# Kernel tuning notes

Hardware: AMD Instinct MI355X
Metric: run time of the kernel (lower is better)

## Reference

```python
import jax, jax.numpy as jnp
import numpy as np

N, LQ, C, M, L, P = 8, 2048, 256, 8, 4, 4
DH = C // M  # 32
LENS = (2048, 1024, 512, 256)


def setup_inputs() -> dict:
    key = jax.random.key(0)
    ks = jax.random.split(key, 8)
    s = 1.0 / np.sqrt(C)
    return {
        "query": jax.random.normal(ks[0], (N, LQ, C), jnp.float32),
        "reference_points": jax.random.uniform(ks[1], (N, LQ, L, 1), jnp.float32),
        "input_flatten": jax.random.normal(ks[2], (N, sum(LENS), C), jnp.float32),
        "temporal_lens": np.array(LENS, np.int64),
        "level_start_index": np.array([0, 2048, 3072, 3584], np.int64),
        "W_off": jax.random.normal(ks[3], (C, M * L * P), jnp.float32) * 0.01,
        "b_off": jax.random.normal(ks[4], (M * L * P,), jnp.float32),
        "W_attn": jax.random.normal(ks[5], (C, M * L * P), jnp.float32) * 0.01,
        "b_attn": jnp.zeros((M * L * P,), jnp.float32),
        "W_val": jax.random.normal(ks[6], (C, C), jnp.float32) * s,
        "b_val": jnp.zeros((C,), jnp.float32),
        "W_out": jax.random.normal(ks[7], (C, C), jnp.float32) * s,
        "b_out": jnp.zeros((C,), jnp.float32),
    }


def _deform_core(value, lens, loc, attn):
    # value: (N, S, M, DH); loc, attn: (N, LQ, M, L, P); loc in normalized [0,1] coords.
    # Equivalent to per-level F.grid_sample (bilinear, zeros padding, align_corners=False)
    # on a 1xT image: pixel position = loc*T - 0.5; the y-coord 0.5 lands exactly on row 0.
    outs = []
    start = 0
    for l, T in enumerate(lens):
        v = value[:, start:start + T].transpose(0, 2, 1, 3)  # (N, M, T, DH)
        start += T
        pos = loc[..., l, :] * T - 0.5                       # (N, LQ, M, P)
        x0f = jnp.floor(pos)
        frac = pos - x0f
        x0 = x0f.astype(jnp.int32)

        def gather(idx):
            i = jnp.clip(idx, 0, T - 1).transpose(0, 2, 1, 3).reshape(N, M, LQ * P, 1)
            return jnp.take_along_axis(v, i, axis=2).reshape(N, M, LQ, P, DH)

        in0 = ((x0 >= 0) & (x0 < T)).astype(value.dtype)
        in1 = ((x0 + 1 >= 0) & (x0 + 1 < T)).astype(value.dtype)
        w0 = ((1.0 - frac) * in0).transpose(0, 2, 1, 3)[..., None]  # (N, M, LQ, P, 1)
        w1 = (frac * in1).transpose(0, 2, 1, 3)[..., None]
        outs.append(gather(x0) * w0 + gather(x0 + 1) * w1)          # (N, M, LQ, P, DH)
    sampled = jnp.stack(outs, axis=3)          # (N, M, LQ, L, P, DH)
    aw = attn.transpose(0, 2, 1, 3, 4)         # (N, M, LQ, L, P)
    return jnp.einsum('nmqlpd,nmqlp->nqmd', sampled, aw).reshape(N, LQ, C)


def reference(query, reference_points, input_flatten, temporal_lens, level_start_index,
              W_off, b_off, W_attn, b_attn, W_val, b_val, W_out, b_out):
    lens = [int(t) for t in np.asarray(temporal_lens)[:L]]  # static per-level lengths
    value = (input_flatten @ W_val + b_val).reshape(N, -1, M, DH)
    off = (query @ W_off + b_off).reshape(N, LQ, M, L, P)
    attn = jax.nn.softmax((query @ W_attn + b_attn).reshape(N, LQ, M, L * P), axis=-1)
    attn = attn.reshape(N, LQ, M, L, P)
    norm = jnp.asarray(lens, query.dtype)                    # offset_normalizer (L,)
    loc = reference_points[:, :, None, :, None, 0] + off / norm[None, None, None, :, None]
    out = _deform_core(value, lens, loc, attn)
    out = out @ W_out + b_out
    return out, loc, attn
```

## Files before the change

### kernel.cpp

```cpp
#include <hip/hip_runtime.h>
#include <hip/hip_bf16.h>
#include <math.h>

#define NB 8
#define LQ 2048
#define SSUM 3840

typedef unsigned short ushort_t;
typedef unsigned int uint_t;
typedef __attribute__((ext_vector_type(8))) short bf16x8;
typedef __attribute__((ext_vector_type(4))) float f32x4;

__device__ __forceinline__ ushort_t f2bf(float f) {
  __hip_bfloat16 h = __float2bfloat16(f);
  return *reinterpret_cast<ushort_t*>(&h);
}
__device__ __forceinline__ uint_t pk2bf(float lo, float hi) {
  float2 t; t.x = lo; t.y = hi;
  __hip_bfloat162 h = __float22bfloat162_rn(t);
  return *reinterpret_cast<uint_t*>(&h);
}
__device__ __forceinline__ float bf2f_lo(uint_t u) {
  union { uint_t u32; float f; } x;
  x.u32 = u << 16;
  return x.f;
}
__device__ __forceinline__ float bf2f_hi(uint_t u) {
  union { uint_t u32; float f; } x;
  x.u32 = u & 0xffff0000u;
  return x.f;
}
__device__ __forceinline__ void ld_lds16(const void* g, void* l) {
  __builtin_amdgcn_global_load_lds(
      (const __attribute__((address_space(1))) void*)g,
      (__attribute__((address_space(3))) void*)l, 16, 0, 0);
}

#define NF4A ((NB * SSUM * 256) / 4)
#define NF4B ((NB * LQ * 256) / 4)

__global__ __launch_bounds__(256) void prologue(
    const float* __restrict__ in_flat, const float* __restrict__ query,
    const float* __restrict__ W_val, const float* __restrict__ W_off,
    const float* __restrict__ W_attn, const float* __restrict__ W_out,
    ushort_t* __restrict__ inflat_bf, ushort_t* __restrict__ query_bf,
    ushort_t* __restrict__ BtVal, ushort_t* __restrict__ BtOA,
    ushort_t* __restrict__ BtOut) {
  const int b = blockIdx.x, t = threadIdx.x;
  if (b < 256) { BtVal[b * 256 + t] = f2bf(W_val[(size_t)t * 256 + b]); return; }
  if (b < 512) { int n = b - 256; BtOut[n * 256 + t] = f2bf(W_out[(size_t)t * 256 + n]); return; }
  if (b < 640) { int n = b - 512; BtOA[n * 256 + t] = f2bf(W_off[(size_t)t * 128 + n]); return; }
  if (b < 768) { int n = b - 640; BtOA[(128 + n) * 256 + t] = f2bf(W_attn[(size_t)t * 128 + n]); return; }
  const int stride = (gridDim.x - 768) * 256;
  for (int i = (b - 768) * 256 + t; i < NF4A + NF4B; i += stride) {
    float4 v;
    if (i < NF4A) v = ((const float4*)in_flat)[i];
    else          v = ((const float4*)query)[i - NF4A];
    uint2 o;
    o.x = pk2bf(v.x, v.y);
    o.y = pk2bf(v.z, v.w);
    if (i < NF4A) *(uint2*)&inflat_bf[(size_t)i * 4] = o;
    else          *(uint2*)&query_bf[(size_t)(i - NF4A) * 4] = o;
  }
}

__global__ __launch_bounds__(256) void gemm_async(
    int job_base,
    const ushort_t* __restrict__ inflat_bf, const ushort_t* __restrict__ query_bf,
    const ushort_t* __restrict__ core,
    const ushort_t* __restrict__ BtVal, const ushort_t* __restrict__ BtOA,
    const ushort_t* __restrict__ BtOut,
    const float* __restrict__ b_val, const float* __restrict__ b_off,
    const float* __restrict__ b_attn, const float* __restrict__ b_out,
    ushort_t* __restrict__ value, float* __restrict__ loc,
    float* __restrict__ attn, float* __restrict__ out) {
  __shared__ ushort_t Ab[2][64][32];
  __shared__ ushort_t Bb[2][128][32];

  const int job = job_base + blockIdx.x;

  const ushort_t* Asrc; const ushort_t* Bt; const float* bias;
  int bm, colbase, cstride;
  ushort_t* Cb = nullptr; float* Cf = nullptr;

  if (job < 960) {
    int cn = job & 1; bm = (job >> 1) * 64;
    Asrc = inflat_bf; Bt = BtVal + cn * 128 * 256;
    bias = b_val + cn * 128; Cb = value; cstride = 256; colbase = cn * 128;
  } else if (job < 1472) {
    int p = job - 960; int cn = p & 1; bm = (p >> 1) * 64;
    Asrc = query_bf; Bt = BtOA + cn * 128 * 256;
    bias = cn ? b_attn : b_off; Cf = cn ? attn : loc; cstride = 128; colbase = 0;
  } else {
    int o = job - 1472; int cn = o & 1; bm = (o >> 1) * 64;
    Asrc = core; Bt = BtOut + cn * 128 * 256;
    bias = b_out + cn * 128; Cf = out; cstride = 256; colbase = cn * 128;
  }

  const int tid = threadIdx.x;
  const int lane = tid & 63;
  const int wv = tid >> 6;
  const int quad = lane >> 4;
  const int l16 = lane & 15;
  const int wm = (wv >> 1) * 32;
  const int wn = (wv & 1) * 64;
  const int srow = lane >> 2;
  const int skb = (lane & 3) * 8;

  f32x4 acc[2][4];
#pragma unroll
  for (int i = 0; i < 2; ++i)
#pragma unroll
    for (int j = 0; j < 4; ++j) acc[i][j] = (f32x4)(0.f);

  auto stage = [&](int db, int k0) {
    ld_lds16(Asrc + (size_t)(bm + wv * 16 + srow) * 256 + k0 + skb,
             &Ab[db][wv * 16 + srow][skb]);
    ld_lds16(Bt + (size_t)(wv * 32 + srow) * 256 + k0 + skb,
             &Bb[db][wv * 32 + srow][skb]);
    ld_lds16(Bt + (size_t)(wv * 32 + 16 + srow) * 256 + k0 + skb,
             &Bb[db][wv * 32 + 16 + srow][skb]);
  };

  stage(0, 0);
#pragma unroll
  for (int it = 0; it < 8; ++it) {
    const int db = it & 1;
    __syncthreads();
    if (it < 7) stage(db ^ 1, (it + 1) * 32);
    bf16x8 af[2], bfr[4];
#pragma unroll
    for (int mi = 0; mi < 2; ++mi)
      af[mi] = *(const bf16x8*)&Ab[db][wm + mi * 16 + l16][quad * 8];
#pragma unroll
    for (int ni = 0; ni < 4; ++ni)
      bfr[ni] = *(const bf16x8*)&Bb[db][wn + ni * 16 + l16][quad * 8];
#pragma unroll
    for (int mi = 0; mi < 2; ++mi)
#pragma unroll
      for (int ni = 0; ni < 4; ++ni)
        acc[mi][ni] = __builtin_amdgcn_mfma_f32_16x16x32_bf16(af[mi], bfr[ni], acc[mi][ni], 0, 0, 0);
  }

#pragma unroll
  for (int ni = 0; ni < 4; ++ni) {
    int lc = wn + ni * 16 + l16;
    float bv = bias[lc];
    int cc = colbase + lc;
#pragma unroll
    for (int mi = 0; mi < 2; ++mi) {
      f32x4 v = acc[mi][ni];
      int rbase = bm + wm + mi * 16 + quad * 4;
#pragma unroll
      for (int r = 0; r < 4; ++r) {
        float o = v[r] + bv;
        size_t idx = (size_t)(rbase + r) * cstride + cc;
        if (Cb) Cb[idx] = f2bf(o);
        else    Cf[idx] = o;
      }
    }
  }
}

__global__ __launch_bounds__(256) void deform_fused(
    const ushort_t* __restrict__ value,
    float* __restrict__ locbuf,
    float* __restrict__ attnbuf,
    const float* __restrict__ refp,
    ushort_t* __restrict__ core) {
  const int tid = threadIdx.x;
  const int nq0 = blockIdx.x * 4;
  const int n = nq0 >> 11;

  __shared__ float slv[512];
  __shared__ float slog[512];
  __shared__ float4 sp[512];

  const float rnorm[4] = {1.f / 2048.f, 1.f / 1024.f, 1.f / 512.f, 1.f / 256.f};
  const int lensA[4] = {2048, 1024, 512, 256};
  const int startsA[4] = {0, 2048, 3072, 3584};

#pragma unroll
  for (int j = 0; j < 2; ++j) {
    int s = tid + j * 256;
    int q = s >> 7;
    int r = s & 127;
    int l = (r >> 2) & 3;
    float lv = refp[(size_t)(nq0 + q) * 4 + l] +
               locbuf[(size_t)nq0 * 128 + s] * rnorm[l];
    locbuf[(size_t)nq0 * 128 + s] = lv;
    slv[s] = lv;
    slog[s] = attnbuf[(size_t)nq0 * 128 + s];
  }
  __syncthreads();

  if (tid < 32) {
    int base = tid * 16;
    float v[16];
#pragma unroll
    for (int i = 0; i < 16; ++i) v[i] = slog[base + i];
    float mx = v[0];
#pragma unroll
    for (int i = 1; i < 16; ++i) mx = fmaxf(mx, v[i]);
    float ssum = 0.f;
#pragma unroll
    for (int i = 0; i < 16; ++i) { v[i] = __expf(v[i] - mx); ssum += v[i]; }
    float rs = 1.f / ssum;
    float* gout = attnbuf + (size_t)nq0 * 128 + base;
#pragma unroll
    for (int i = 0; i < 16; ++i) {
      float pv = v[i] * rs;
      slog[base + i] = pv;
      gout[i] = pv;
    }
  }
  __syncthreads();

#pragma unroll
  for (int j = 0; j < 2; ++j) {
    int s = tid + j * 256;
    int q = s >> 7;
    int r = s & 127;
    int m = r >> 4;
    int lp = r & 15;
    int l = lp >> 2;
    int T = lensA[l];
    float lv = slv[s];
    float aw = slog[s];
    float pos = lv * (float)T - 0.5f;
    float x0f = floorf(pos);
    float fr = pos - x0f;
    int x0 = (int)x0f;
    float w0 = ((unsigned)x0 < (unsigned)T) ? (1.f - fr) * aw : 0.f;
    float w1 = ((unsigned)(x0 + 1) < (unsigned)T) ? fr * aw : 0.f;
    int i0 = min(max(x0, 0), T - 1);
    int i1 = min(max(x0 + 1, 0), T - 1);
    float4 pr;
    pr.x = w0;
    pr.y = w1;
    pr.z = __int_as_float((startsA[l] + i0) * 256);
    pr.w = __int_as_float((startsA[l] + i1) * 256);
    sp[q * 128 + lp * 8 + m] = pr;
  }
  __syncthreads();

  const int q = tid >> 6;
  const int t64 = tid & 63;
  const int m = t64 >> 3;
  const int g = t64 & 7;
  const ushort_t* vbase = value + (size_t)n * (SSUM * 256) + m * 32 + g * 4;

  float a0 = 0.f, a1 = 0.f, a2 = 0.f, a3 = 0.f;
#pragma unroll
  for (int lp = 0; lp < 16; ++lp) {
    float4 pr = sp[q * 128 + lp * 8 + m];
    int o0 = __float_as_int(pr.z);
    int o1 = __float_as_int(pr.w);
    uint2 u0 = *(const uint2*)(vbase + o0);
    uint2 u1 = *(const uint2*)(vbase + o1);
    a0 += pr.x * bf2f_lo(u0.x) + pr.y * bf2f_lo(u1.x);
    a1 += pr.x * bf2f_hi(u0.x) + pr.y * bf2f_hi(u1.x);
    a2 += pr.x * bf2f_lo(u0.y) + pr.y * bf2f_lo(u1.y);
    a3 += pr.x * bf2f_hi(u0.y) + pr.y * bf2f_hi(u1.y);
  }
  uint2 outp;
  outp.x = (uint_t)f2bf(a0) | ((uint_t)f2bf(a1) << 16);
  outp.y = (uint_t)f2bf(a2) | ((uint_t)f2bf(a3) << 16);
  *(uint2*)&core[(size_t)(nq0 + q) * 256 + m * 32 + g * 4] = outp;
}

extern "C" void kernel_launch(void* const* d_in, const int* in_sizes, int n_in,
                              void* d_out, int out_size, void* d_ws, size_t ws_size,
                              hipStream_t stream) {
  const float* query    = (const float*)d_in[0];
  const float* refpts   = (const float*)d_in[1];
  const float* in_flat  = (const float*)d_in[2];
  const float* W_off  = (const float*)d_in[5];
  const float* b_off  = (const float*)d_in[6];
  const float* W_attn = (const float*)d_in[7];
  const float* b_attn = (const float*)d_in[8];
  const float* W_val  = (const float*)d_in[9];
  const float* b_val  = (const float*)d_in[10];
  const float* W_out  = (const float*)d_in[11];
  const float* b_out  = (const float*)d_in[12];

  float* out  = (float*)d_out;
  float* loc  = out + (size_t)NB * LQ * 256;
  float* attn = loc + (size_t)NB * LQ * 128;

  ushort_t* value     = (ushort_t*)d_ws;
  ushort_t* inflat_bf = value + (size_t)NB * SSUM * 256;
  ushort_t* query_bf  = inflat_bf + (size_t)NB * SSUM * 256;
  ushort_t* core      = query_bf;
  ushort_t* BtVal     = query_bf + (size_t)NB * LQ * 256;
  ushort_t* BtOA      = BtVal + 65536;
  ushort_t* BtOut     = BtOA + 65536;

  const int Mq = NB * LQ;

  prologue<<<768 + 2048, 256, 0, stream>>>(
      in_flat, query, W_val, W_off, W_attn, W_out,
      inflat_bf, query_bf, BtVal, BtOA, BtOut);

  gemm_async<<<1472, 256, 0, stream>>>(
      0, inflat_bf, query_bf, core, BtVal, BtOA, BtOut,
      b_val, b_off, b_attn, b_out, value, loc, attn, out);

  deform_fused<<<Mq / 4, 256, 0, stream>>>(value, loc, attn, refpts, core);

  gemm_async<<<512, 256, 0, stream>>>(
      1472, inflat_bf, query_bf, core, BtVal, BtOA, BtOut,
      b_val, b_off, b_attn, b_out, value, loc, attn, out);
}
```

Baseline: 174.5 us.

## Fuse fp32-to-bf16 activation conversion into GEMM with direct register loads

Removes the separate bulk conversion pass that wrote bf16 copies of input_flatten and query. The GEMM now reads fp32 activations straight from global memory and converts them to bf16 in registers. It also drops the LDS double-buffered async staging, so every wave loads its own A and B fragments from global memory. This saves one full read and write of the activations, but it loses LDS data sharing between waves, so global and L2 traffic for B and A rises, and the loads are no longer overlapped with compute.

Result: slower. 199.9 us (+14.6%).

```diff
diff --git a/kernel.cpp b/kernel.cpp
--- a/kernel.cpp
+++ b/kernel.cpp
@@ -30,43 +30,22 @@
   x.u32 = u & 0xffff0000u;
   return x.f;
 }
-__device__ __forceinline__ void ld_lds16(const void* g, void* l) {
-  __builtin_amdgcn_global_load_lds(
-      (const __attribute__((address_space(1))) void*)g,
-      (__attribute__((address_space(3))) void*)l, 16, 0, 0);
-}
-
-#define NF4A ((NB * SSUM * 256) / 4)
-#define NF4B ((NB * LQ * 256) / 4)
-
-__global__ __launch_bounds__(256) void prologue(
-    const float* __restrict__ in_flat, const float* __restrict__ query,
+
+__global__ __launch_bounds__(256) void prep(
     const float* __restrict__ W_val, const float* __restrict__ W_off,
     const float* __restrict__ W_attn, const float* __restrict__ W_out,
-    ushort_t* __restrict__ inflat_bf, ushort_t* __restrict__ query_bf,
     ushort_t* __restrict__ BtVal, ushort_t* __restrict__ BtOA,
     ushort_t* __restrict__ BtOut) {
   const int b = blockIdx.x, t = threadIdx.x;
   if (b < 256) { BtVal[b * 256 + t] = f2bf(W_val[(size_t)t * 256 + b]); return; }
   if (b < 512) { int n = b - 256; BtOut[n * 256 + t] = f2bf(W_out[(size_t)t * 256 + n]); return; }
   if (b < 640) { int n = b - 512; BtOA[n * 256 + t] = f2bf(W_off[(size_t)t * 128 + n]); return; }
-  if (b < 768) { int n = b - 640; BtOA[(128 + n) * 256 + t] = f2bf(W_attn[(size_t)t * 128 + n]); return; }
-  const int stride = (gridDim.x - 768) * 256;
-  for (int i = (b - 768) * 256 + t; i < NF4A + NF4B; i += stride) {
-    float4 v;
-    if (i < NF4A) v = ((const float4*)in_flat)[i];
-    else          v = ((const float4*)query)[i - NF4A];
-    uint2 o;
-    o.x = pk2bf(v.x, v.y);
-    o.y = pk2bf(v.z, v.w);
-    if (i < NF4A) *(uint2*)&inflat_bf[(size_t)i * 4] = o;
-    else          *(uint2*)&query_bf[(size_t)(i - NF4A) * 4] = o;
-  }
-}
-
-__global__ __launch_bounds__(256) void gemm_async(
+  int n = b - 640; BtOA[(128 + n) * 256 + t] = f2bf(W_attn[(size_t)t * 128 + n]);
+}
+
+__global__ __launch_bounds__(256) void gemm_reg(
     int job_base,
-    const ushort_t* __restrict__ inflat_bf, const ushort_t* __restrict__ query_bf,
+    const float* __restrict__ in_flat, const float* __restrict__ query,
     const ushort_t* __restrict__ core,
     const ushort_t* __restrict__ BtVal, const ushort_t* __restrict__ BtOA,
     const ushort_t* __restrict__ BtOut,
@@ -74,26 +53,25 @@
     const float* __restrict__ b_attn, const float* __restrict__ b_out,
     ushort_t* __restrict__ value, float* __restrict__ loc,
     float* __restrict__ attn, float* __restrict__ out) {
-  __shared__ ushort_t Ab[2][64][32];
-  __shared__ ushort_t Bb[2][128][32];
-
   const int job = job_base + blockIdx.x;
 
-  const ushort_t* Asrc; const ushort_t* Bt; const float* bias;
+  const float* Afp = nullptr;
+  const ushort_t* Abf = nullptr;
+  const ushort_t* Bt; const float* bias;
   int bm, colbase, cstride;
   ushort_t* Cb = nullptr; float* Cf = nullptr;
 
   if (job < 960) {
     int cn = job & 1; bm = (job >> 1) * 64;
-    Asrc = inflat_bf; Bt = BtVal + cn * 128 * 256;
+    Afp = in_flat; Bt = BtVal + cn * 128 * 256;
     bias = b_val + cn * 128; Cb = value; cstride = 256; colbase = cn * 128;
   } else if (job < 1472) {
     int p = job - 960; int cn = p & 1; bm = (p >> 1) * 64;
-    Asrc = query_bf; Bt = BtOA + cn * 128 * 256;
+    Afp = query; Bt = BtOA + cn * 128 * 256;
     bias = cn ? b_attn : b_off; Cf = cn ? attn : loc; cstride = 128; colbase = 0;
   } else {
     int o = job - 1472; int cn = o & 1; bm = (o >> 1) * 64;
-    Asrc = core; Bt = BtOut + cn * 128 * 256;
+    Abf = core; Bt = BtOut + cn * 128 * 256;
     bias = b_out + cn * 128; Cf = out; cstride = 256; colbase = cn * 128;
   }
 
@@ -104,8 +82,13 @@
   const int l16 = lane & 15;
   const int wm = (wv >> 1) * 32;
   const int wn = (wv & 1) * 64;
-  const int srow = lane >> 2;
-  const int skb = (lane & 3) * 8;
+
+  const size_t arow0 = (size_t)(bm + wm + l16) * 256 + quad * 8;
+  const size_t arow1 = arow0 + 16 * 256;
+  const ushort_t* bcol[4];
+#pragma unroll
+  for (int ni = 0; ni < 4; ++ni)
+    bcol[ni] = Bt + (size_t)(wn + ni * 16 + l16) * 256 + quad * 8;
 
   f32x4 acc[2][4];
 #pragma unroll
@@ -113,28 +96,32 @@
 #pragma unroll
     for (int j = 0; j < 4; ++j) acc[i][j] = (f32x4)(0.f);
 
-  auto stage = [&](int db, int k0) {
-    ld_lds16(Asrc + (size_t)(bm + wv * 16 + srow) * 256 + k0 + skb,
-             &Ab[db][wv * 16 + srow][skb]);
-    ld_lds16(Bt + (size_t)(wv * 32 + srow) * 256 + k0 + skb,
-             &Bb[db][wv * 32 + srow][skb]);
-    ld_lds16(Bt + (size_t)(wv * 32 + 16 + srow) * 256 + k0 + skb,
-             &Bb[db][wv * 32 + 16 + srow][skb]);
-  };
-
-  stage(0, 0);
-#pragma unroll
-  for (int it = 0; it < 8; ++it) {
-    const int db = it & 1;
-    __syncthreads();
-    if (it < 7) stage(db ^ 1, (it + 1) * 32);
+  union cvt_t { uint4 u; bf16x8 v; };
+
+#pragma unroll
+  for (int kk = 0; kk < 8; ++kk) {
+    const int k0 = kk * 32;
     bf16x8 af[2], bfr[4];
-#pragma unroll
-    for (int mi = 0; mi < 2; ++mi)
-      af[mi] = *(const bf16x8*)&Ab[db][wm + mi * 16 + l16][quad * 8];
+    if (Afp) {
+#pragma unroll
+      for (int mi = 0; mi < 2; ++mi) {
+        const float* gp = Afp + (mi ? arow1 : arow0) + k0;
+        float4 f0 = *(const float4*)gp;
+        float4 f1 = *(const float4*)(gp + 4);
+        cvt_t c;
+        c.u.x = pk2bf(f0.x, f0.y);
+        c.u.y = pk2bf(f0.z, f0.w);
+        c.u.z = pk2bf(f1.x, f1.y);
+        c.u.w = pk2bf(f1.z, f1.w);
+        af[mi] = c.v;
+      }
+    } else {
+      af[0] = *(const bf16x8*)(Abf + arow0 + k0);
+      af[1] = *(const bf16x8*)(Abf + arow1 + k0);
+    }
 #pragma unroll
     for (int ni = 0; ni < 4; ++ni)
-      bfr[ni] = *(const bf16x8*)&Bb[db][wn + ni * 16 + l16][quad * 8];
+      bfr[ni] = *(const bf16x8*)(bcol[ni] + k0);
 #pragma unroll
     for (int mi = 0; mi < 2; ++mi)
 #pragma unroll
@@ -288,27 +275,23 @@
   float* loc  = out + (size_t)NB * LQ * 256;
   float* attn = loc + (size_t)NB * LQ * 128;
 
-  ushort_t* value     = (ushort_t*)d_ws;
-  ushort_t* inflat_bf = value + (size_t)NB * SSUM * 256;
-  ushort_t* query_bf  = inflat_bf + (size_t)NB * SSUM * 256;
-  ushort_t* core      = query_bf;
-  ushort_t* BtVal     = query_bf + (size_t)NB * LQ * 256;
-  ushort_t* BtOA      = BtVal + 65536;
-  ushort_t* BtOut     = BtOA + 65536;
+  ushort_t* value = (ushort_t*)d_ws;
+  ushort_t* core  = value + (size_t)NB * SSUM * 256;
+  ushort_t* BtVal = core + (size_t)NB * LQ * 256;
+  ushort_t* BtOA  = BtVal + 65536;
+  ushort_t* BtOut = BtOA + 65536;
 
   const int Mq = NB * LQ;
 
-  prologue<<<768 + 2048, 256, 0, stream>>>(
-      in_flat, query, W_val, W_off, W_attn, W_out,
-      inflat_bf, query_bf, BtVal, BtOA, BtOut);
-
-  gemm_async<<<1472, 256, 0, stream>>>(
-      0, inflat_bf, query_bf, core, BtVal, BtOA, BtOut,
+  prep<<<768, 256, 0, stream>>>(W_val, W_off, W_attn, W_out, BtVal, BtOA, BtOut);
+
+  gemm_reg<<<1472, 256, 0, stream>>>(
+      0, in_flat, query, core, BtVal, BtOA, BtOut,
       b_val, b_off, b_attn, b_out, value, loc, attn, out);
 
   deform_fused<<<Mq / 4, 256, 0, stream>>>(value, loc, attn, refpts, core);
 
-  gemm_async<<<512, 256, 0, stream>>>(
-      1472, inflat_bf, query_bf, core, BtVal, BtOA, BtOut,
+  gemm_reg<<<512, 256, 0, stream>>>(
+      1472, in_flat, query, core, BtVal, BtOA, BtOut,
       b_val, b_off, b_attn, b_out, value, loc, attn, out);
 }
```
